# Kernel optimization log

Measured on AMD Instinct MI355X. Metric: run time of the kernel, lower is better.

The kernel has to match this reference:

```python
import jax, jax.numpy as jnp
import numpy as np

BATCH, IN, OUT = 8192, 4096, 4096


def setup_inputs() -> dict:
    key = jax.random.key(0)
    k1, k2, k3 = jax.random.split(key, 3)
    x = jax.random.normal(k1, (BATCH, IN), dtype=jnp.float32)
    weight = jax.random.normal(k2, (OUT, IN), dtype=jnp.float32)
    bias = jax.random.normal(k3, (OUT,), dtype=jnp.float32)
    return {"x": x, "weight": weight, "bias": bias}


def reference(x, weight, bias):
    # Binarize weights/bias with sign (matches torch.sign: sign(0)=0), then fp32 GEMM + bias add.
    w = jnp.sign(weight)            # [OUT, IN], values in {-1, 0, +1}
    b = jnp.sign(bias)              # [OUT]
    return jnp.dot(x, w.T) + b[None, :]   # [BATCH, OUT]
```

## Files before the change

### kernel.cpp

```cpp
#include <hip/hip_runtime.h>
#include <stdint.h>
#include <stddef.h>


#define MDIM 8192
#define NDIM 4096
#define KDIM 4096

typedef __attribute__((ext_vector_type(8))) short bf16x8;
typedef __attribute__((ext_vector_type(4))) float f32x4;

__device__ __forceinline__ short f2bf(float f) {
  union { float f; unsigned u; } a; a.f = f;
  unsigned r = a.u + 0x7FFFu + ((a.u >> 16) & 1u);
  return (short)(r >> 16);
}

__device__ __forceinline__ float fsign(float x) {
  return (x > 0.f) ? 1.f : ((x < 0.f) ? -1.f : 0.f);
}

__device__ __forceinline__ short signbf(float x) {
  return (x > 0.f) ? (short)0x3F80 : ((x < 0.f) ? (short)0xBF80 : (short)0);
}

__device__ __forceinline__ void gl_lds16(const void* g, void* l) {
  __builtin_amdgcn_global_load_lds(
      (const __attribute__((address_space(1))) unsigned*)g,
      (__attribute__((address_space(3))) unsigned*)l,
      16, 0, 0);
}


__global__ void cvt_x_kernel(const float* __restrict__ x, short* __restrict__ o) {
  int i = blockIdx.x * blockDim.x + threadIdx.x;
  float4 v = ((const float4*)x)[i];
  short4 s;
  s.x = f2bf(v.x); s.y = f2bf(v.y); s.z = f2bf(v.z); s.w = f2bf(v.w);
  ((short4*)o)[i] = s;
}

__global__ void cvt_w_kernel(const float* __restrict__ w, short* __restrict__ o) {
  int i = blockIdx.x * blockDim.x + threadIdx.x;
  float4 v = ((const float4*)w)[i];
  short4 s;
  s.x = signbf(v.x); s.y = signbf(v.y); s.z = signbf(v.z); s.w = signbf(v.w);
  ((short4*)o)[i] = s;
}


__global__ __launch_bounds__(256) void gemm_ws(
    const short* __restrict__ A,
    const short* __restrict__ B,
    const float* __restrict__ bias,
    float* __restrict__ C) {
  __shared__ short As[128 * 32];
  __shared__ short Bs[128 * 32];

  const int t    = threadIdx.x;
  const int lane = t & 63;
  const int wm   = (t >> 6) >> 1;
  const int wn   = (t >> 6) & 1;

  const int bm = blockIdx.y * 128;
  const int bn = blockIdx.x * 128;

  f32x4 acc[4][4] = {};

  const int srow = t >> 2;
  const int scol = (t & 3) << 3;

  const short* aA0 = A + (size_t)(bm + srow) * KDIM + scol;
  const short* aA1 = A + (size_t)(bm + 64 + srow) * KDIM + scol;
  const short* aB0 = B + (size_t)(bn + srow) * KDIM + scol;
  const short* aB1 = B + (size_t)(bn + 64 + srow) * KDIM + scol;

  char* ldsA0 = (char*)As + t * 16;
  char* ldsA1 = (char*)As + 4096 + t * 16;
  char* ldsB0 = (char*)Bs + t * 16;
  char* ldsB1 = (char*)Bs + 4096 + t * 16;

  const int fr  = lane & 15;
  const int fkB = (lane >> 4) << 4;

  for (int k0 = 0; k0 < KDIM; k0 += 32) {
    gl_lds16(aA0 + k0, ldsA0);
    gl_lds16(aA1 + k0, ldsA1);
    gl_lds16(aB0 + k0, ldsB0);
    gl_lds16(aB1 + k0, ldsB1);
    __syncthreads();

    bf16x8 af[4], bfr[4];
#pragma unroll
    for (int i = 0; i < 4; ++i) {
      af[i]  = *(const bf16x8*)((const char*)As + (wm * 64 + i * 16 + fr) * 64 + fkB);
      bfr[i] = *(const bf16x8*)((const char*)Bs + (wn * 64 + i * 16 + fr) * 64 + fkB);
    }
#pragma unroll
    for (int i = 0; i < 4; ++i)
#pragma unroll
      for (int j = 0; j < 4; ++j)
        acc[i][j] = __builtin_amdgcn_mfma_f32_16x16x32_bf16(af[i], bfr[j], acc[i][j], 0, 0, 0);
    __syncthreads();
  }

  const int row0 = bm + wm * 64 + ((lane >> 4) << 2);
  const int col0 = bn + wn * 64 + (lane & 15);
#pragma unroll
  for (int j = 0; j < 4; ++j) {
    const int gc = col0 + j * 16;
    const float bs = fsign(bias[gc]);
#pragma unroll
    for (int i = 0; i < 4; ++i) {
      float* cp = C + (size_t)(row0 + i * 16) * NDIM + gc;
#pragma unroll
      for (int r = 0; r < 4; ++r)
        cp[(size_t)r * NDIM] = acc[i][j][r] + bs;
    }
  }
}


__global__ __launch_bounds__(256) void gemm_fused(
    const float* __restrict__ A,
    const float* __restrict__ W,
    const float* __restrict__ bias,
    float* __restrict__ C) {
  __shared__ short As[128 * 32];
  __shared__ short Bs[128 * 32];

  const int t    = threadIdx.x;
  const int lane = t & 63;
  const int wm   = (t >> 6) >> 1;
  const int wn   = (t >> 6) & 1;

  const int bm = blockIdx.y * 128;
  const int bn = blockIdx.x * 128;

  f32x4 acc[4][4] = {};

  const int srow = t >> 1;
  const int scol = (t & 1) << 4;

  const float* pA = A + (size_t)(bm + srow) * KDIM + scol;
  const float* pW = W + (size_t)(bn + srow) * KDIM + scol;
  short* sA = As + srow * 32 + scol;
  short* sB = Bs + srow * 32 + scol;

  const int fr  = lane & 15;
  const int fkB = (lane >> 4) << 4;

  for (int k0 = 0; k0 < KDIM; k0 += 32) {
    float4 va[4], vb[4];
#pragma unroll
    for (int q = 0; q < 4; ++q) {
      va[q] = *(const float4*)(pA + k0 + q * 4);
      vb[q] = *(const float4*)(pW + k0 + q * 4);
    }
    __syncthreads();
    bf16x8 ca, cb;
#pragma unroll
    for (int q = 0; q < 4; ++q) {
      ca[q * 2 + 0] = 0;
    }
    short va_s[16], vb_s[16];
#pragma unroll
    for (int q = 0; q < 4; ++q) {
      va_s[q * 4 + 0] = f2bf(va[q].x); va_s[q * 4 + 1] = f2bf(va[q].y);
      va_s[q * 4 + 2] = f2bf(va[q].z); va_s[q * 4 + 3] = f2bf(va[q].w);
      vb_s[q * 4 + 0] = signbf(vb[q].x); vb_s[q * 4 + 1] = signbf(vb[q].y);
      vb_s[q * 4 + 2] = signbf(vb[q].z); vb_s[q * 4 + 3] = signbf(vb[q].w);
    }
#pragma unroll
    for (int e = 0; e < 8; ++e) { ca[e] = va_s[e]; cb[e] = vb_s[e]; }
    *(bf16x8*)(sA) = ca;
    *(bf16x8*)(sB) = cb;
#pragma unroll
    for (int e = 0; e < 8; ++e) { ca[e] = va_s[8 + e]; cb[e] = vb_s[8 + e]; }
    *(bf16x8*)(sA + 8) = ca;
    *(bf16x8*)(sB + 8) = cb;
    __syncthreads();

    bf16x8 af[4], bfr[4];
#pragma unroll
    for (int i = 0; i < 4; ++i) {
      af[i]  = *(const bf16x8*)((const char*)As + (wm * 64 + i * 16 + fr) * 64 + fkB);
      bfr[i] = *(const bf16x8*)((const char*)Bs + (wn * 64 + i * 16 + fr) * 64 + fkB);
    }
#pragma unroll
    for (int i = 0; i < 4; ++i)
#pragma unroll
      for (int j = 0; j < 4; ++j)
        acc[i][j] = __builtin_amdgcn_mfma_f32_16x16x32_bf16(af[i], bfr[j], acc[i][j], 0, 0, 0);
  }
  __syncthreads();

  const int row0 = bm + wm * 64 + ((lane >> 4) << 2);
  const int col0 = bn + wn * 64 + (lane & 15);
#pragma unroll
  for (int j = 0; j < 4; ++j) {
    const int gc = col0 + j * 16;
    const float bs = fsign(bias[gc]);
#pragma unroll
    for (int i = 0; i < 4; ++i) {
      float* cp = C + (size_t)(row0 + i * 16) * NDIM + gc;
#pragma unroll
      for (int r = 0; r < 4; ++r)
        cp[(size_t)r * NDIM] = acc[i][j][r] + bs;
    }
  }
}

extern "C" void kernel_launch(void* const* d_in, const int* in_sizes, int n_in,
                              void* d_out, int out_size, void* d_ws, size_t ws_size,
                              hipStream_t stream) {
  const float* x    = (const float*)d_in[0];
  const float* w    = (const float*)d_in[1];
  const float* bias = (const float*)d_in[2];
  float* out = (float*)d_out;

  const size_t xb_bytes = (size_t)MDIM * KDIM * 2;
  const size_t wb_bytes = (size_t)NDIM * KDIM * 2;

  dim3 grid(NDIM / 128, MDIM / 128);

  if (ws_size >= xb_bytes + wb_bytes) {
    short* xb = (short*)d_ws;
    short* wb = (short*)((char*)d_ws + xb_bytes);
    cvt_x_kernel<<<(MDIM * (KDIM / 4)) / 256, 256, 0, stream>>>(x, xb);
    cvt_w_kernel<<<(NDIM * (KDIM / 4)) / 256, 256, 0, stream>>>(w, wb);
    gemm_ws<<<grid, 256, 0, stream>>>(xb, wb, bias, out);
  } else {
    gemm_fused<<<grid, 256, 0, stream>>>(x, w, bias, out);
  }
}
```

Baseline: 556.8 us.

## Fuse x fp32-to-fp16 conversion into GEMM, switch to fp16 MFMA with swizzled LDS

Drops the separate x-to-bf16 conversion kernel and its workspace round trip. The GEMM now loads fp32 x tiles directly into LDS and converts them to fp16 in registers with cvt_pkrtz. Weights are pre-signed into fp16 ±1/0, and the MFMA switches from bf16 to f16. XOR swizzling is added to the LDS layouts to avoid bank conflicts. In exchange, LDS traffic for A doubles and there is per-iteration conversion work, and fp16 with round-toward-zero gives a different error profile (more mantissa, less range).

```diff
diff --git a/kernel.cpp b/kernel.cpp
--- a/kernel.cpp
+++ b/kernel.cpp
@@ -7,21 +7,28 @@
 #define NDIM 4096
 #define KDIM 4096
 
+typedef __attribute__((ext_vector_type(8))) _Float16 f16x8;
+typedef __attribute__((ext_vector_type(2))) __fp16 pk16x2;
+typedef __attribute__((ext_vector_type(4))) float f32x4;
 typedef __attribute__((ext_vector_type(8))) short bf16x8;
-typedef __attribute__((ext_vector_type(4))) float f32x4;
+
+union frag_u {
+  f16x8 v;
+  pk16x2 p[4];
+};
+
+__device__ __forceinline__ float fsign(float x) {
+  return (x > 0.f) ? 1.f : ((x < 0.f) ? -1.f : 0.f);
+}
+
+__device__ __forceinline__ short signh(float x) {
+  return (x > 0.f) ? (short)0x3C00 : ((x < 0.f) ? (short)0xBC00 : (short)0);
+}
 
 __device__ __forceinline__ short f2bf(float f) {
   union { float f; unsigned u; } a; a.f = f;
   unsigned r = a.u + 0x7FFFu + ((a.u >> 16) & 1u);
   return (short)(r >> 16);
-}
-
-__device__ __forceinline__ float fsign(float x) {
-  return (x > 0.f) ? 1.f : ((x < 0.f) ? -1.f : 0.f);
-}
-
-__device__ __forceinline__ short signbf(float x) {
-  return (x > 0.f) ? (short)0x3F80 : ((x < 0.f) ? (short)0xBF80 : (short)0);
 }
 
 __device__ __forceinline__ void gl_lds16(const void* g, void* l) {
@@ -32,29 +39,21 @@
 }
 
 
-__global__ void cvt_x_kernel(const float* __restrict__ x, short* __restrict__ o) {
-  int i = blockIdx.x * blockDim.x + threadIdx.x;
-  float4 v = ((const float4*)x)[i];
-  short4 s;
-  s.x = f2bf(v.x); s.y = f2bf(v.y); s.z = f2bf(v.z); s.w = f2bf(v.w);
-  ((short4*)o)[i] = s;
-}
-
 __global__ void cvt_w_kernel(const float* __restrict__ w, short* __restrict__ o) {
   int i = blockIdx.x * blockDim.x + threadIdx.x;
   float4 v = ((const float4*)w)[i];
   short4 s;
-  s.x = signbf(v.x); s.y = signbf(v.y); s.z = signbf(v.z); s.w = signbf(v.w);
+  s.x = signh(v.x); s.y = signh(v.y); s.z = signh(v.z); s.w = signh(v.w);
   ((short4*)o)[i] = s;
 }
 
 
-__global__ __launch_bounds__(256) void gemm_ws(
-    const short* __restrict__ A,
+__global__ __launch_bounds__(256) void gemm_fx(
+    const float* __restrict__ A,
     const short* __restrict__ B,
     const float* __restrict__ bias,
     float* __restrict__ C) {
-  __shared__ short As[128 * 32];
+  __shared__ float As[128 * 32];
   __shared__ short Bs[128 * 32];
 
   const int t    = threadIdx.x;
@@ -67,40 +66,59 @@
 
   f32x4 acc[4][4] = {};
 
-  const int srow = t >> 2;
-  const int scol = (t & 3) << 3;
-
-  const short* aA0 = A + (size_t)(bm + srow) * KDIM + scol;
-  const short* aA1 = A + (size_t)(bm + 64 + srow) * KDIM + scol;
-  const short* aB0 = B + (size_t)(bn + srow) * KDIM + scol;
-  const short* aB1 = B + (size_t)(bn + 64 + srow) * KDIM + scol;
-
-  char* ldsA0 = (char*)As + t * 16;
-  char* ldsA1 = (char*)As + 4096 + t * 16;
-  char* ldsB0 = (char*)Bs + t * 16;
-  char* ldsB1 = (char*)Bs + 4096 + t * 16;
-
-  const int fr  = lane & 15;
-  const int fkB = (lane >> 4) << 4;
+  const float* gA[4]; void* lA[4];
+#pragma unroll
+  for (int q = 0; q < 4; ++q) {
+    const int c = q * 256 + t;
+    const int row = c >> 3, g = c & 7;
+    const int gg = g ^ (row & 7);
+    gA[q] = A + (size_t)(bm + row) * KDIM + gg * 4;
+    lA[q] = (char*)As + c * 16;
+  }
+  const short* gB[2]; void* lB[2];
+#pragma unroll
+  for (int q = 0; q < 2; ++q) {
+    const int c = q * 256 + t;
+    const int row = c >> 2, g = c & 3;
+    const int gg = g ^ ((row >> 1) & 3);
+    gB[q] = B + (size_t)(bn + row) * KDIM + gg * 8;
+    lB[q] = (char*)Bs + c * 16;
+  }
+
+  const int fr = lane & 15;
+  const int kg = lane >> 4;
 
   for (int k0 = 0; k0 < KDIM; k0 += 32) {
-    gl_lds16(aA0 + k0, ldsA0);
-    gl_lds16(aA1 + k0, ldsA1);
-    gl_lds16(aB0 + k0, ldsB0);
-    gl_lds16(aB1 + k0, ldsB1);
-    __syncthreads();
-
-    bf16x8 af[4], bfr[4];
-#pragma unroll
-    for (int i = 0; i < 4; ++i) {
-      af[i]  = *(const bf16x8*)((const char*)As + (wm * 64 + i * 16 + fr) * 64 + fkB);
-      bfr[i] = *(const bf16x8*)((const char*)Bs + (wn * 64 + i * 16 + fr) * 64 + fkB);
+#pragma unroll
+    for (int q = 0; q < 4; ++q) gl_lds16(gA[q] + k0, lA[q]);
+#pragma unroll
+    for (int q = 0; q < 2; ++q) gl_lds16(gB[q] + k0, lB[q]);
+    __syncthreads();
+
+    f16x8 af[4], bfr[4];
+#pragma unroll
+    for (int i = 0; i < 4; ++i) {
+      const int r = wm * 64 + i * 16 + fr;
+      const char* rb = (const char*)As + r * 128;
+      f32x4 lo = *(const f32x4*)(rb + (((2 * kg)     ^ (r & 7)) << 4));
+      f32x4 hi = *(const f32x4*)(rb + (((2 * kg + 1) ^ (r & 7)) << 4));
+      frag_u u;
+      u.p[0] = __builtin_amdgcn_cvt_pkrtz(lo[0], lo[1]);
+      u.p[1] = __builtin_amdgcn_cvt_pkrtz(lo[2], lo[3]);
+      u.p[2] = __builtin_amdgcn_cvt_pkrtz(hi[0], hi[1]);
+      u.p[3] = __builtin_amdgcn_cvt_pkrtz(hi[2], hi[3]);
+      af[i] = u.v;
+    }
+#pragma unroll
+    for (int j = 0; j < 4; ++j) {
+      const int r = wn * 64 + j * 16 + fr;
+      bfr[j] = *(const f16x8*)((const char*)Bs + r * 64 + ((kg ^ ((r >> 1) & 3)) << 4));
     }
 #pragma unroll
     for (int i = 0; i < 4; ++i)
 #pragma unroll
       for (int j = 0; j < 4; ++j)
-        acc[i][j] = __builtin_amdgcn_mfma_f32_16x16x32_bf16(af[i], bfr[j], acc[i][j], 0, 0, 0);
+        acc[i][j] = __builtin_amdgcn_mfma_f32_16x16x32_f16(af[i], bfr[j], acc[i][j], 0, 0, 0);
     __syncthreads();
   }
 
@@ -133,7 +151,6 @@
   const int lane = t & 63;
   const int wm   = (t >> 6) >> 1;
   const int wn   = (t >> 6) & 1;
-
   const int bm = blockIdx.y * 128;
   const int bn = blockIdx.x * 128;
 
@@ -141,7 +158,6 @@
 
   const int srow = t >> 1;
   const int scol = (t & 1) << 4;
-
   const float* pA = A + (size_t)(bm + srow) * KDIM + scol;
   const float* pW = W + (size_t)(bn + srow) * KDIM + scol;
   short* sA = As + srow * 32 + scol;
@@ -158,19 +174,15 @@
       vb[q] = *(const float4*)(pW + k0 + q * 4);
     }
     __syncthreads();
-    bf16x8 ca, cb;
-#pragma unroll
-    for (int q = 0; q < 4; ++q) {
-      ca[q * 2 + 0] = 0;
-    }
     short va_s[16], vb_s[16];
 #pragma unroll
     for (int q = 0; q < 4; ++q) {
       va_s[q * 4 + 0] = f2bf(va[q].x); va_s[q * 4 + 1] = f2bf(va[q].y);
       va_s[q * 4 + 2] = f2bf(va[q].z); va_s[q * 4 + 3] = f2bf(va[q].w);
-      vb_s[q * 4 + 0] = signbf(vb[q].x); vb_s[q * 4 + 1] = signbf(vb[q].y);
-      vb_s[q * 4 + 2] = signbf(vb[q].z); vb_s[q * 4 + 3] = signbf(vb[q].w);
-    }
+      vb_s[q * 4 + 0] = f2bf(fsign(vb[q].x)); vb_s[q * 4 + 1] = f2bf(fsign(vb[q].y));
+      vb_s[q * 4 + 2] = f2bf(fsign(vb[q].z)); vb_s[q * 4 + 3] = f2bf(fsign(vb[q].w));
+    }
+    bf16x8 ca, cb;
 #pragma unroll
     for (int e = 0; e < 8; ++e) { ca[e] = va_s[e]; cb[e] = vb_s[e]; }
     *(bf16x8*)(sA) = ca;
@@ -219,17 +231,14 @@
   const float* bias = (const float*)d_in[2];
   float* out = (float*)d_out;
 
-  const size_t xb_bytes = (size_t)MDIM * KDIM * 2;
   const size_t wb_bytes = (size_t)NDIM * KDIM * 2;
 
   dim3 grid(NDIM / 128, MDIM / 128);
 
-  if (ws_size >= xb_bytes + wb_bytes) {
-    short* xb = (short*)d_ws;
-    short* wb = (short*)((char*)d_ws + xb_bytes);
-    cvt_x_kernel<<<(MDIM * (KDIM / 4)) / 256, 256, 0, stream>>>(x, xb);
+  if (ws_size >= wb_bytes) {
+    short* wb = (short*)d_ws;
     cvt_w_kernel<<<(NDIM * (KDIM / 4)) / 256, 256, 0, stream>>>(w, wb);
-    gemm_ws<<<grid, 256, 0, stream>>>(xb, wb, bias, out);
+    gemm_fx<<<grid, 256, 0, stream>>>(x, wb, bias, out);
   } else {
     gemm_fused<<<grid, 256, 0, stream>>>(x, w, bias, out);
   }
```

Result: slower. 658.9 us (+18.3%).
